# Performance work log

Hardware: AMD Instinct MI355X
Metric: run time of the kernel (lower is better)

The kernel has to match this reference:

```python
import jax, jax.numpy as jnp
import numpy as np

D = 128; T = 128; E = 100; H = 2
B = 2048; N0 = 3 * B; K0 = 5; N1 = N0 * K0; K1 = 10
NN = 200000; M = 4096; MSG = 2 * D + E + T  # 484


def t2v(t, w, b):
    # Time2Vec: cos(t * w + b), output [..., T]
    return jnp.cos(t[..., None] * w + b)


def gru_cell(x, h, Wih, bih, Whh, bhh):
    gi = x @ Wih.T + bih
    gh = h @ Whh.T + bhh
    ir, iz, inn = jnp.split(gi, 3, axis=-1)
    hr, hz, hn = jnp.split(gh, 3, axis=-1)
    r = jax.nn.sigmoid(ir + hr)
    u = jax.nn.sigmoid(iz + hz)
    n = jnp.tanh(inn + r * hn)
    return (1.0 - u) * n + u * h


def temporal_attn(node_feat, time_feat, edge_feat, nbr_feat, nbr_time_feat, mask,
                  Wq, bq, Wk, bk, Wv, bv, Wo, bo):
    N = node_feat.shape[0]
    q = (jnp.concatenate([node_feat, time_feat], -1) @ Wq + bq).reshape(N, H, D // H)
    kin = jnp.concatenate([nbr_feat, edge_feat, nbr_time_feat], -1)  # [N, K, D+E+T]
    k = (kin @ Wk + bk).reshape(N, -1, H, D // H)
    v = (kin @ Wv + bv).reshape(N, -1, H, D // H)
    s = jnp.einsum('nhd,nkhd->nhk', q, k) / jnp.sqrt(jnp.asarray(D // H, q.dtype))
    s = jnp.where(mask[:, None, :] > 0, s, jnp.asarray(-1e9, s.dtype))
    a = jax.nn.softmax(s, axis=-1)
    hout = jnp.einsum('nhk,nkhd->nhd', a, v).reshape(N, D)
    return jax.nn.relu(jnp.concatenate([hout, node_feat], -1) @ Wo + bo)


def setup_inputs() -> dict:
    key = jax.random.key(0)
    ks = jax.random.split(key, 60)
    it = iter(range(60))
    nx = lambda: ks[next(it)]
    p = lambda shape: jax.random.normal(nx(), shape, jnp.float32) * 0.05
    inp = dict(memory=p((NN, D)), time_w=p((T,)), time_b=p((T,)),
               gru_Wih=p((3 * D, MSG)), gru_bih=p((3 * D,)),
               gru_Whh=p((3 * D, D)), gru_bhh=p((3 * D,)))
    for l in (0, 1):
        inp['Wq%d' % l] = p((D + T, D)); inp['bq%d' % l] = p((D,))
        inp['Wk%d' % l] = p((D + E + T, D)); inp['bk%d' % l] = p((D,))
        inp['Wv%d' % l] = p((D + E + T, D)); inp['bv%d' % l] = p((D,))
        inp['Wo%d' % l] = p((2 * D, D)); inp['bo%d' % l] = p((D,))
    inp.update(lp_Ws=p((D, D)), lp_bs=p((D,)), lp_Wd=p((D, D)), lp_bd=p((D,)),
               lp_Wo=p((D, 1)), lp_bo=p((1,)))
    inp['msgs'] = jax.random.normal(nx(), (M, MSG), jnp.float32)
    inp['times0'] = jax.random.uniform(nx(), (N0,), jnp.float32) * 100.0 + 100.0
    inp['nbr_times0'] = inp['times0'][:, None] - jax.random.uniform(nx(), (N0, K0), jnp.float32) * 100.0
    inp['nbr_feats0'] = jax.random.normal(nx(), (N0, K0, E), jnp.float32)
    inp['times1'] = jax.random.uniform(nx(), (N1,), jnp.float32) * 100.0 + 100.0
    inp['nbr_times1'] = inp['times1'][:, None] - jax.random.uniform(nx(), (N1, K1), jnp.float32) * 100.0
    inp['nbr_feats1'] = jax.random.normal(nx(), (N1, K1, E), jnp.float32)
    inp['msg_nids'] = jax.random.permutation(nx(), NN)[:M].astype(jnp.int32)
    inp['seed0'] = jax.random.randint(nx(), (N0,), 0, NN, jnp.int32)
    inp['seed1'] = jax.random.randint(nx(), (N1,), 0, NN, jnp.int32)
    inp['nbr_local0'] = (N0 + jax.random.randint(nx(), (N0, K0), 0, N1)).astype(jnp.int32)
    inp['nbr_mask0'] = jax.random.randint(nx(), (N0, K0), 0, 2, jnp.int32).at[:, 0].set(1)
    inp['nbr_mask1'] = jax.random.randint(nx(), (N1, K1), 0, 2, jnp.int32).at[:, 0].set(1)
    inp['src_local'] = jax.random.randint(nx(), (B,), 0, N0, jnp.int32)
    inp['dst_local'] = jax.random.randint(nx(), (B,), 0, N0, jnp.int32)
    inp['neg_local'] = jax.random.randint(nx(), (B,), 0, N0, jnp.int32)
    return inp


def reference(memory, time_w, time_b, gru_Wih, gru_bih, gru_Whh, gru_bhh,
              Wq0, bq0, Wk0, bk0, Wv0, bv0, Wo0, bo0,
              Wq1, bq1, Wk1, bk1, Wv1, bv1, Wo1, bo1,
              lp_Ws, lp_bs, lp_Wd, lp_bd, lp_Wo, lp_bo,
              msgs, times0, nbr_times0, nbr_feats0, times1, nbr_times1, nbr_feats1,
              msg_nids, seed0, seed1, nbr_local0, nbr_mask0, nbr_mask1,
              src_local, dst_local, neg_local):
    # GRU memory update on aggregated messages (get_updated_memory)
    mem = memory.at[msg_nids].set(
        gru_cell(msgs, memory[msg_nids], gru_Wih, gru_bih, gru_Whh, gru_bhh))
    z = jnp.zeros((N0 + N1, D), jnp.float32)
    # hop 1 (outermost): neighbor node features are zeros
    tf1 = t2v(jnp.zeros((N1,), jnp.float32), time_w, time_b)
    ntf1 = t2v(times1[:, None] - nbr_times1, time_w, time_b)
    out1 = temporal_attn(mem[seed1], tf1, nbr_feats1,
                         jnp.zeros((N1, K1, D), jnp.float32), ntf1, nbr_mask1,
                         Wq1, bq1, Wk1, bk1, Wv1, bv1, Wo1, bo1)
    z = z.at[N0 + jnp.arange(N1)].set(out1)
    # hop 0: gather neighbor embeddings from hop-1 results
    tf0 = t2v(jnp.zeros((N0,), jnp.float32), time_w, time_b)
    ntf0 = t2v(times0[:, None] - nbr_times0, time_w, time_b)
    out0 = temporal_attn(mem[seed0], tf0, nbr_feats0, z[nbr_local0], ntf0, nbr_mask0,
                         Wq0, bq0, Wk0, bk0, Wv0, bv0, Wo0, bo0)
    z = z.at[jnp.arange(N0)].set(out0)
    z_src, z_dst, z_neg = z[src_local], z[dst_local], z[neg_local]

    def link_pred(a, c):
        hh = jax.nn.relu(a @ lp_Ws + lp_bs + c @ lp_Wd + lp_bd)
        return jax.nn.sigmoid(hh @ lp_Wo + lp_bo).ravel()

    return link_pred(z_src, z_dst), link_pred(z_src, z_neg)
```

## Files before the change

kernel.cpp:

```cpp
#include <hip/hip_runtime.h>
#include <math.h>

#define D    128
#define TT   128
#define E    100
#define NHD  2
#define BSZ  2048
#define N0C  6144
#define K0C  5
#define N1C  30720
#define K1C  10
#define NNC  200000
#define MC   4096
#define MSG  484
#define KIN  356
#define GK   612
#define GKP  616
#define GN   512

typedef __attribute__((ext_vector_type(8))) short short8v;
typedef __attribute__((ext_vector_type(4))) float f32x4;

__device__ __forceinline__ float sigmoidf_(float x){ return 1.f/(1.f+__expf(-x)); }
__device__ __forceinline__ unsigned short f2b(float f){
    unsigned int x = __float_as_uint(f);
    unsigned int r = (x + 0x7fffu + ((x>>16)&1u)) >> 16;
    return (unsigned short)r;
}
__device__ __forceinline__ float b2f(unsigned short u){
    return __uint_as_float(((unsigned int)u)<<16);
}

__global__ void k_pre_small(const float* time_b,
                            const float* Wq0,const float* bq0,const float* Wq1,const float* bq1,
                            const float* bv0,const float* Wo0,const float* bo0,
                            const float* bv1,const float* Wo1,const float* bo1,
                            float* qc0, float* qc1, float* cb0, float* cb1){
    __shared__ float cosb[TT];
    int j = threadIdx.x;
    cosb[j] = cosf(time_b[j]);
    __syncthreads();
    float a0=bq0[j], a1=bq1[j];
    for(int t=0;t<TT;++t){ a0 += cosb[t]*Wq0[(D+t)*D + j]; a1 += cosb[t]*Wq1[(D+t)*D + j]; }
    qc0[j]=a0; qc1[j]=a1;
    float c0=bo0[j], c1=bo1[j];
    for(int jp=0;jp<D;++jp){ c0 += bv0[jp]*Wo0[jp*D + j]; c1 += bv1[jp]*Wo1[jp*D + j]; }
    cb0[j]=c0; cb1[j]=c1;
}

__global__ void k_wf(const float* Wq,const float* Wk,const float* bk,const float* qc,
                     unsigned short* WF, float* cF, int cmin){
    int span = 356 - cmin;
    int hstr = span + 4;
    int width = 2*hstr;
    int idx = blockIdx.x;
    int h = idx / hstr; int cl = idx % hstr;
    int k = threadIdx.x;
    if(cl > span){
        WF[(size_t)k*width + idx] = (unsigned short)0;
        if(k==0) cF[idx] = 0.f;
        return;
    }
    int c = cmin + cl;
    float a = 0.f;
    for(int d=0; d<64; ++d){
        float wkv = (c < KIN) ? Wk[c*D + h*64+d] : bk[h*64+d];
        a += Wq[k*D + h*64+d] * wkv;
    }
    WF[(size_t)k*width + idx] = f2b(a);
    if(k==0){
        float s=0.f;
        for(int d=0; d<64; ++d){
            float wkv = (c < KIN) ? Wk[c*D + h*64+d] : bk[h*64+d];
            s += qc[h*64+d]*wkv;
        }
        cF[idx] = s;
    }
}

__global__ void k_bcat(const float* Wv, const float* Wo, unsigned short* Bcat, int cmin){
    int span = KIN - cmin; int rows = 2*span;
    int r = blockIdx.x; int j = threadIdx.x;
    float a;
    if(r < rows){
        int h = r/span; int c = cmin + (r - h*span);
        a = 0.f;
        for(int d=0; d<64; ++d) a += Wv[c*D + h*64+d] * Wo[(h*64+d)*D + j];
    } else {
        a = Wo[(size_t)(D + (r - rows))*D + j];
    }
    Bcat[(size_t)r*D + j] = f2b(a);
}

__global__ __launch_bounds__(256) void k_gruB(const float* Wih, const float* Whh, unsigned short* B){
    __shared__ float tile[64][65];
    int rb = blockIdx.x*64;
    int jb = blockIdx.y*64;
    int t = threadIdx.x;
    int rr = t&63, jj0 = t>>6;
    #pragma unroll
    for(int i=0;i<16;++i){
        int jj = jj0 + i*4;
        int j = jb + jj; int r = rb + rr;
        float v = 0.f;
        if(r < GK){
            if(j < 256)      v = (r<MSG)? Wih[(size_t)j*MSG+r] : Whh[(size_t)j*D + (r-MSG)];
            else if(j < 384) v = (r<MSG)? Wih[(size_t)j*MSG+r] : 0.f;
            else             v = (r<MSG)? 0.f : Whh[(size_t)(j-128)*D + (r-MSG)];
        }
        tile[jj][rr] = v;
    }
    __syncthreads();
    int jw = t&63, rr0 = t>>6;
    #pragma unroll
    for(int i=0;i<16;++i){
        int rr2 = rr0 + i*4;
        int r = rb + rr2;
        if(r < GK) B[(size_t)r*GN + jb + jw] = f2b(tile[jw][rr2]);
    }
}
__global__ void k_gruBias(const float* bih, const float* bhh, float* bias){
    int j = threadIdx.x + blockIdx.x*256;
    if(j >= GN) return;
    float v;
    if(j < 256)      v = bih[j] + bhh[j];
    else if(j < 384) v = bih[j];
    else             v = bhh[j-128];
    bias[j] = v;
}
__global__ void k_acvt(const float* msgs, const float* memory, const int* msg_nids,
                       unsigned short* ab, float* hprevf){
    int i = blockIdx.x*256 + threadIdx.x;
    if(i >= MC*GKP) return;
    int row = i / GKP; int c = i - row*GKP;
    float v;
    if(c < MSG) v = msgs[(size_t)row*MSG + c];
    else if(c < GK){ int d = c-MSG; v = memory[(size_t)msg_nids[row]*D + d]; hprevf[row*D+d] = v; }
    else v = 0.f;
    ab[i] = f2b(v);
}
__global__ void k_gates3(const float* part, const float* bias, const float* hprevf, float* upd){
    int i = blockIdx.x*256 + threadIdx.x;
    if(i >= MC*D) return;
    int row = i>>7, d = i&127;
    const float* p = part + (size_t)row*GN;
    const size_t S = (size_t)MC*GN;
    float gr = p[d]     + p[S+d]     + p[2*S+d]     + bias[d];
    float gu = p[128+d] + p[S+128+d] + p[2*S+128+d] + bias[128+d];
    float gi = p[256+d] + p[S+256+d] + p[2*S+256+d] + bias[256+d];
    float gh = p[384+d] + p[S+384+d] + p[2*S+384+d] + bias[384+d];
    float r = sigmoidf_(gr);
    float u = sigmoidf_(gu);
    float n = tanhf(gi + r*gh);
    upd[i] = (1.f-u)*n + u*hprevf[i];
}

__global__ void k_map_init(int* map){ int i = blockIdx.x*256+threadIdx.x; if(i<NNC) map[i] = -1; }
__global__ void k_map_scatter(const int* msg_nids, int* map){
    int i = blockIdx.x*256+threadIdx.x; if(i<MC) map[msg_nids[i]] = i;
}

__global__ void k_gatherf(const int* seed1,const int* seed0,const int* map,
                          const float* memory,const float* upd,
                          unsigned short* hb1, unsigned short* acat1,
                          unsigned short* hb0, unsigned short* acat0){
    int i = blockIdx.x*256 + threadIdx.x;
    const int total1 = N1C*D;
    int li; const int* seed; unsigned short* hb; unsigned short* acat; int ldav, hoff;
    if(i < total1){ li=i; seed=seed1; hb=hb1; acat=acat1; ldav=584; hoff=456; }
    else { li = i - total1; if(li >= N0C*D) return; seed=seed0; hb=hb0; acat=acat0; ldav=840; hoff=712; }
    int row = li>>7, c = li&127;
    int sid = seed[row];
    int mi = map[sid];
    float v = (mi>=0) ? upd[(size_t)mi*D + c] : memory[(size_t)sid*D + c];
    unsigned short u = f2b(v);
    hb[li] = u;
    acat[(size_t)row*ldav + hoff + c] = u;
}

template<int BM, int SPLITK, bool RELU, bool OUTF32>
__global__ __launch_bounds__(256) void k_gmm(const unsigned short* A, int lda,
                                             const unsigned short* B, int ldb,
                                             const float* bias, void* Cp, int ldc,
                                             int K, int N, int M){
    constexpr int ASTR = 72;
    constexpr int BSTR = 72;
    constexpr int RPW = BM/4;
    constexpr int RT  = RPW/16;
    constexpr int AIT = BM/32;
    __shared__ unsigned short As[BM*ASTR];
    __shared__ unsigned short Bs[64*BSTR];
    int t = threadIdx.x;
    int wave = t>>6, lane = t&63;
    int l15 = lane&15, l4 = lane>>4;
    int m0 = blockIdx.y*BM, n0 = blockIdx.x*64;
    int ntiles = (K+63)>>6;
    int tbeg, tend;
    if(SPLITK==1){ tbeg=0; tend=ntiles; }
    else {
        int tper = (ntiles + SPLITK-1)/SPLITK;
        tbeg = blockIdx.z*tper;
        tend = min(ntiles, tbeg+tper);
    }
    f32x4 acc[RT][4];
    #pragma unroll
    for(int rt=0;rt<RT;++rt)
        #pragma unroll
        for(int ct=0;ct<4;++ct) acc[rt][ct] = (f32x4){0.f,0.f,0.f,0.f};

    uint4 apre[AIT]; unsigned short bpre[16];
    auto loadA = [&](int kt){
        int k0 = kt<<6;
        #pragma unroll
        for(int i=0;i<AIT;++i){
            int idx = t + i*256;
            int row = idx>>3; int kc = (idx&7)*8;
            uint4 v = {0u,0u,0u,0u};
            if(k0+kc < K) v = *(const uint4*)(A + (size_t)(m0+row)*lda + k0 + kc);
            apre[i] = v;
        }
    };
    auto loadB = [&](int kt){
        int k0 = kt<<6;
        int n = t&63; int kb = (t>>6)*16;
        int ng = n0+n;
        #pragma unroll
        for(int j=0;j<16;++j){
            int kg = k0 + kb + j;
            bpre[j] = (kg<K && ng<N) ? B[(size_t)kg*ldb + ng] : (unsigned short)0;
        }
    };
    auto stash = [&](){
        #pragma unroll
        for(int i=0;i<AIT;++i){
            int idx = t + i*256;
            int row = idx>>3; int kc = (idx&7)*8;
            *(uint4*)&As[row*ASTR + kc] = apre[i];
        }
        int n = t&63; int kb = (t>>6)*16;
        #pragma unroll
        for(int j=0;j<16;++j) Bs[n*BSTR + kb + j] = bpre[j];
    };

    loadA(tbeg); loadB(tbeg);
    for(int kt=tbeg; kt<tend; ++kt){
        stash();
        __syncthreads();
        if(kt+1 < tend){ loadA(kt+1); loadB(kt+1); }
        #pragma unroll
        for(int kk=0; kk<64; kk+=32){
            short8v bfr[4];
            #pragma unroll
            for(int ct=0;ct<4;++ct)
                bfr[ct] = *(const short8v*)&Bs[(ct*16+l15)*BSTR + kk + l4*8];
            #pragma unroll
            for(int rt=0;rt<RT;++rt){
                short8v afr = *(const short8v*)&As[(wave*RPW + rt*16 + l15)*ASTR + kk + l4*8];
                #pragma unroll
                for(int ct=0;ct<4;++ct)
                    acc[rt][ct] = __builtin_amdgcn_mfma_f32_16x16x32_bf16(afr, bfr[ct], acc[rt][ct], 0,0,0);
            }
        }
        __syncthreads();
    }
    #pragma unroll
    for(int rt=0;rt<RT;++rt){
        #pragma unroll
        for(int ct=0;ct<4;++ct){
            int col = n0 + ct*16 + l15;
            if(col < N){
                #pragma unroll
                for(int r=0;r<4;++r){
                    int row = m0 + wave*RPW + rt*16 + l4*4 + r;
                    if(SPLITK==1){
                        float v = acc[rt][ct][r] + bias[col];
                        if(RELU) v = fmaxf(v, 0.f);
                        if(OUTF32) ((float*)Cp)[(size_t)row*ldc + col] = v;
                        else ((unsigned short*)Cp)[(size_t)row*ldc + col] = f2b(v);
                    } else {
                        ((float*)Cp)[((size_t)blockIdx.z*M + row)*ldc + col] = acc[rt][ct][r];
                    }
                }
            }
        }
    }
}

template<int SPL, bool RELU, bool OUTF32>
__global__ void k_kred(const float* part, int M, int N, const float* bias, void* out){
    int i = blockIdx.x*256 + threadIdx.x;
    if(i >= M*N) return;
    int col = i & (N-1);
    float v = bias[col];
    #pragma unroll
    for(int z=0;z<SPL;++z) v += part[(size_t)z*M*N + i];
    if(RELU) v = fmaxf(v, 0.f);
    if(OUTF32) ((float*)out)[i] = v;
    else ((unsigned short*)out)[i] = f2b(v);
}

template<int K, int CMIN, int S4, int NPW>
__global__ __launch_bounds__(256) void k_attn(const unsigned short* qwb,
    unsigned short* avout, int ldav,
    const float* times, const float* nbr_times, const float* nbr_feats,
    const int* nbr_mask, const int* nbr_local, const unsigned short* zbuf,
    const float* time_w, const float* time_b){
    constexpr int SPAN = KIN - CMIN;
    constexpr int QSTR = SPAN + 4;
    constexpr int QLD  = 2*QSTR;
    int wv = blockIdx.x*4 + (threadIdx.x>>6);
    int lane = threadIdx.x & 63;

    float4 tw4[S4], tb4[S4];
    #pragma unroll
    for(int s=0;s<S4;++s){
        int c = CMIN + s*256 + lane*4;
        if(c >= D+E && c < KIN){
            tw4[s] = *(const float4*)(time_w + (c-(D+E)));
            tb4[s] = *(const float4*)(time_b + (c-(D+E)));
        } else {
            tw4[s] = make_float4(0.f,0.f,0.f,0.f);
            tb4[s] = make_float4(0.f,0.f,0.f,0.f);
        }
    }

    for(int i=0;i<NPW;++i){
        int n = wv*NPW + i;
        const unsigned short* qrow = qwb + (size_t)n*QLD;
        float tval = (lane<K) ? nbr_times[(size_t)n*K + lane] : 0.f;
        int   mval = (lane<K) ? nbr_mask [(size_t)n*K + lane] : 0;
        int   nlv  = (CMIN==0 && lane<K) ? nbr_local[(size_t)n*K + lane] : 0;
        float tn = times[n];

        float4 qw4[NHD][S4]; float qb[NHD];
        #pragma unroll
        for(int h=0;h<NHD;++h){
            qb[h] = b2f(qrow[h*QSTR + SPAN]);
            #pragma unroll
            for(int s=0;s<S4;++s){
                int cl = s*256 + lane*4;
                float4 v = make_float4(0.f,0.f,0.f,0.f);
                if(cl < SPAN){
                    uint2 w = *(const uint2*)(qrow + h*QSTR + cl);
                    v.x = __uint_as_float(w.x<<16);
                    v.y = __uint_as_float(w.x & 0xffff0000u);
                    v.z = __uint_as_float(w.y<<16);
                    v.w = __uint_as_float(w.y & 0xffff0000u);
                }
                qw4[h][s] = v;
            }
        }

        float4 kin4[K][S4];
        float sval[NHD][K];
        unsigned int actmask = 0;
        #pragma unroll
        for(int k=0;k<K;++k){
            int mk = __shfl(mval, k);
            if(mk > 0){
                actmask |= (1u<<k);
                float dt = tn - __shfl(tval, k);
                const float* ef = nbr_feats + (size_t)(n*K+k)*E;
                const unsigned short* zf = (CMIN==0) ?
                    (zbuf + (size_t)(__shfl(nlv,k) - N0C)*D) : (const unsigned short*)0;
                float p0=0.f, p1=0.f;
                #pragma unroll
                for(int s=0;s<S4;++s){
                    int c = CMIN + s*256 + lane*4;
                    float4 kv = make_float4(0.f,0.f,0.f,0.f);
                    if(c < KIN){
                        if(CMIN==0 && c < D){
                            uint2 w = *(const uint2*)(zf + c);
                            kv.x = __uint_as_float(w.x<<16);
                            kv.y = __uint_as_float(w.x & 0xffff0000u);
                            kv.z = __uint_as_float(w.y<<16);
                            kv.w = __uint_as_float(w.y & 0xffff0000u);
                        } else if(c < D+E){
                            kv = *(const float4*)(ef + (c-D));
                        } else {
                            kv.x = __cosf(dt*tw4[s].x + tb4[s].x);
                            kv.y = __cosf(dt*tw4[s].y + tb4[s].y);
                            kv.z = __cosf(dt*tw4[s].z + tb4[s].z);
                            kv.w = __cosf(dt*tw4[s].w + tb4[s].w);
                        }
                    }
                    kin4[k][s] = kv;
                    p0 += kv.x*qw4[0][s].x + kv.y*qw4[0][s].y + kv.z*qw4[0][s].z + kv.w*qw4[0][s].w;
                    p1 += kv.x*qw4[1][s].x + kv.y*qw4[1][s].y + kv.z*qw4[1][s].z + kv.w*qw4[1][s].w;
                }
                #pragma unroll
                for(int off=32; off; off>>=1){ p0 += __shfl_xor(p0, off); p1 += __shfl_xor(p1, off); }
                sval[0][k] = (p0 + qb[0])*0.125f;
                sval[1][k] = (p1 + qb[1])*0.125f;
            } else {
                #pragma unroll
                for(int s=0;s<S4;++s) kin4[k][s] = make_float4(0.f,0.f,0.f,0.f);
                sval[0][k] = -1e9f;
                sval[1][k] = -1e9f;
            }
        }
        #pragma unroll
        for(int h=0;h<NHD;++h){
            float mx = -1e30f;
            #pragma unroll
            for(int k=0;k<K;++k) mx = fmaxf(mx, sval[h][k]);
            float z=0.f;
            #pragma unroll
            for(int k=0;k<K;++k){ float e = __expf(sval[h][k]-mx); sval[h][k]=e; z+=e; }
            float inv = 1.f/z;
            #pragma unroll
            for(int k=0;k<K;++k) sval[h][k]*=inv;
        }
        #pragma unroll
        for(int h=0;h<NHD;++h)
          #pragma unroll
          for(int s=0;s<S4;++s){
            int cl = s*256 + lane*4;
            if(cl < SPAN){
                float v0=0.f,v1=0.f,v2=0.f,v3=0.f;
                #pragma unroll
                for(int k=0;k<K;++k){
                    if(actmask & (1u<<k)){
                        float a = sval[h][k];
                        v0 += a*kin4[k][s].x; v1 += a*kin4[k][s].y;
                        v2 += a*kin4[k][s].z; v3 += a*kin4[k][s].w;
                    }
                }
                uint2 o;
                o.x = (unsigned int)f2b(v0) | ((unsigned int)f2b(v1)<<16);
                o.y = (unsigned int)f2b(v2) | ((unsigned int)f2b(v3)<<16);
                *(uint2*)(avout + (size_t)n*ldav + h*SPAN + cl) = o;
            }
          }
    }
}

__global__ __launch_bounds__(128) void k_linkpred(const float* z0,
      const int* src,const int* dst,const int* neg,
      const float* Ws,const float* bs,const float* Wd,const float* bd,
      const float* Wo,const float* bo, float* out){
    __shared__ float zs[D], zd[D], zn[D];
    __shared__ float red[4];
    int b = blockIdx.x; int d = threadIdx.x;
    zs[d] = z0[(size_t)src[b]*D + d];
    zd[d] = z0[(size_t)dst[b]*D + d];
    zn[d] = z0[(size_t)neg[b]*D + d];
    __syncthreads();
    float ss=0.f, sdd=0.f, snn=0.f;
    for(int c=0;c<D;++c){
        float w1 = Ws[c*D + d], w2 = Wd[c*D + d];
        ss  += zs[c]*w1; sdd += zd[c]*w2; snn += zn[c]*w2;
    }
    float bb = bs[d] + bd[d];
    float h1 = fmaxf(ss + sdd + bb, 0.f);
    float h2 = fmaxf(ss + snn + bb, 0.f);
    float w = Wo[d];
    float v1 = h1*w, v2 = h2*w;
    #pragma unroll
    for(int off=32; off; off>>=1){ v1 += __shfl_xor(v1,off); v2 += __shfl_xor(v2,off); }
    int wid = d>>6;
    if((d&63)==0){ red[wid*2]=v1; red[wid*2+1]=v2; }
    __syncthreads();
    if(d==0){
        out[b]       = sigmoidf_(red[0]+red[2] + bo[0]);
        out[BSZ + b] = sigmoidf_(red[1]+red[3] + bo[0]);
    }
}

extern "C" void kernel_launch(void* const* d_in, const int* in_sizes, int n_in,
                              void* d_out, int out_size, void* d_ws, size_t ws_size,
                              hipStream_t stream) {
    const float* memory  = (const float*)d_in[0];
    const float* time_w  = (const float*)d_in[1];
    const float* time_b  = (const float*)d_in[2];
    const float* gWih    = (const float*)d_in[3];
    const float* gbih    = (const float*)d_in[4];
    const float* gWhh    = (const float*)d_in[5];
    const float* gbhh    = (const float*)d_in[6];
    const float* Wq0=(const float*)d_in[7],  *bq0=(const float*)d_in[8];
    const float* Wk0=(const float*)d_in[9],  *bk0=(const float*)d_in[10];
    const float* Wv0=(const float*)d_in[11], *bv0=(const float*)d_in[12];
    const float* Wo0=(const float*)d_in[13], *bo0=(const float*)d_in[14];
    const float* Wq1=(const float*)d_in[15], *bq1=(const float*)d_in[16];
    const float* Wk1=(const float*)d_in[17], *bk1=(const float*)d_in[18];
    const float* Wv1=(const float*)d_in[19], *bv1=(const float*)d_in[20];
    const float* Wo1=(const float*)d_in[21], *bo1=(const float*)d_in[22];
    const float* lpWs=(const float*)d_in[23], *lpbs=(const float*)d_in[24];
    const float* lpWd=(const float*)d_in[25], *lpbd=(const float*)d_in[26];
    const float* lpWo=(const float*)d_in[27], *lpbo=(const float*)d_in[28];
    const float* msgs    = (const float*)d_in[29];
    const float* times0  = (const float*)d_in[30];
    const float* ntimes0 = (const float*)d_in[31];
    const float* nfeats0 = (const float*)d_in[32];
    const float* times1  = (const float*)d_in[33];
    const float* ntimes1 = (const float*)d_in[34];
    const float* nfeats1 = (const float*)d_in[35];
    const int* msg_nids  = (const int*)d_in[36];
    const int* seed0     = (const int*)d_in[37];
    const int* seed1     = (const int*)d_in[38];
    const int* nbr_local0= (const int*)d_in[39];
    const int* nbr_mask0 = (const int*)d_in[40];
    const int* nbr_mask1 = (const int*)d_in[41];
    const int* src       = (const int*)d_in[42];
    const int* dst       = (const int*)d_in[43];
    const int* neg       = (const int*)d_in[44];

    char* ws = (char*)d_ws;
    size_t off = 0;
    auto alloc = [&](size_t bytes)->char*{
        char* p = ws + off;
        off += (bytes + 255) & ~(size_t)255;
        return p;
    };
    int*   map   = (int*)  alloc((size_t)NNC*4);
    float* upd   = (float*)alloc((size_t)MC*D*4);
    unsigned short* hb1   = (unsigned short*)alloc((size_t)N1C*D*2);
    unsigned short* qwb1  = (unsigned short*)alloc((size_t)N1C*464*2);
    unsigned short* acat1 = (unsigned short*)alloc((size_t)N1C*584*2);
    unsigned short* zb1   = (unsigned short*)alloc((size_t)N1C*D*2);
    unsigned short* hb0   = (unsigned short*)alloc((size_t)N0C*D*2);
    unsigned short* qwb0  = (unsigned short*)alloc((size_t)N0C*720*2);
    unsigned short* acat0 = (unsigned short*)alloc((size_t)N0C*840*2);
    float* z0    = (float*)alloc((size_t)N0C*D*4);
    float* qc0   = (float*)alloc(512);
    float* qc1   = (float*)alloc(512);
    float* cb0   = (float*)alloc(512);
    float* cb1   = (float*)alloc(512);
    unsigned short* WFb0 = (unsigned short*)alloc((size_t)D*720*2);
    unsigned short* WFb1 = (unsigned short*)alloc((size_t)D*464*2);
    float* cF0   = (float*)alloc((size_t)720*4);
    float* cF1   = (float*)alloc((size_t)464*4);
    unsigned short* Bcat1 = (unsigned short*)alloc((size_t)584*D*2);
    unsigned short* Bcat0 = (unsigned short*)alloc((size_t)840*D*2);
    unsigned short* gA    = (unsigned short*)alloc((size_t)MC*GKP*2);
    unsigned short* gB    = (unsigned short*)alloc((size_t)GK*GN*2);
    float* gBias = (float*)alloc((size_t)GN*4);
    float* hprevf= (float*)alloc((size_t)MC*D*4);
    float* part  = (float*)alloc((size_t)2*N1C*D*4);
    float* outp = (float*)d_out;

    k_pre_small<<<1,128,0,stream>>>(time_b, Wq0,bq0,Wq1,bq1, bv0,Wo0,bo0, bv1,Wo1,bo1,
                                    qc0,qc1,cb0,cb1);
    k_wf<<<720,128,0,stream>>>(Wq0,Wk0,bk0,qc0, WFb0,cF0, 0);
    k_wf<<<464,128,0,stream>>>(Wq1,Wk1,bk1,qc1, WFb1,cF1, 128);
    k_bcat<<<584,128,0,stream>>>(Wv1, Wo1, Bcat1, 128);
    k_bcat<<<840,128,0,stream>>>(Wv0, Wo0, Bcat0, 0);
    k_gruB<<<dim3(10,8),256,0,stream>>>(gWih, gWhh, gB);
    k_gruBias<<<2,256,0,stream>>>(gbih, gbhh, gBias);

    k_map_init<<<(NNC+255)/256,256,0,stream>>>(map);
    k_map_scatter<<<MC/256,256,0,stream>>>(msg_nids, map);
    k_acvt<<<(MC*GKP+255)/256,256,0,stream>>>(msgs, memory, msg_nids, gA, hprevf);
    k_gmm<128,3,false,true><<<dim3(GN/64, MC/128, 3),256,0,stream>>>(gA,GKP, gB,GN, gBias, part,GN, GK, GN, MC);
    k_gates3<<<(MC*D+255)/256,256,0,stream>>>(part, gBias, hprevf, upd);

    k_gatherf<<<((N1C+N0C)*D)/256,256,0,stream>>>(seed1, seed0, map, memory, upd,
                                                  hb1, acat1, hb0, acat0);

    k_gmm<128,1,false,false><<<dim3(8,  N1C/128),256,0,stream>>>(hb1,128, WFb1,464, cF1, qwb1,464, 128, 464, N1C);
    k_gmm<128,1,false,false><<<dim3(12, N0C/128),256,0,stream>>>(hb0,128, WFb0,720, cF0, qwb0,720, 128, 720, N0C);

    k_attn<K1C,128,1,2><<<N1C/8,256,0,stream>>>(qwb1, acat1, 584, times1, ntimes1, nfeats1,
                                                nbr_mask1, (const int*)0, (const unsigned short*)0,
                                                time_w, time_b);
    k_gmm<128,2,true,false><<<dim3(2, N1C/128, 2),256,0,stream>>>(acat1,584, Bcat1,D, cb1, part,D, 584, D, N1C);
    k_kred<2,true,false><<<(N1C*D+255)/256,256,0,stream>>>(part, N1C, D, cb1, zb1);

    k_attn<K0C,0,2,1><<<N0C/4,256,0,stream>>>(qwb0, acat0, 840, times0, ntimes0, nfeats0,
                                              nbr_mask0, nbr_local0, zb1,
                                              time_w, time_b);
    k_gmm<64,4,true,true><<<dim3(2, N0C/64, 4),256,0,stream>>>(acat0,840, Bcat0,D, cb0, part,D, 840, D, N0C);
    k_kred<4,true,true><<<(N0C*D+255)/256,256,0,stream>>>(part, N0C, D, cb0, z0);

    k_linkpred<<<BSZ,128,0,stream>>>(z0, src,dst,neg, lpWs,lpbs,lpWd,lpbd, lpWo,lpbo, outp);
}
```

Measured before the change: 599.2 us.

## Batch neighbor loads and shuffle reductions in attention kernel, drop mask branches

Restructures the temporal attention kernel so that mask, time and neighbor-index values for all K neighbors are read up front. All key vectors are then gathered before the dot products, and the cross-lane reductions for every neighbor run together. Per-neighbor mask branches go away: masked neighbors are computed and then zeroed through the -1e9 softmax score. Hop 1 now uses one node per wave with twice the blocks; `__restrict__` and readfirstlane are added. The aim is more memory-level and instruction-level parallelism to hide gather latency, at the cost of more registers and extra loads for masked neighbors, whose indices may point to invalid memory.

```diff
diff --git a/kernel.cpp b/kernel.cpp
--- a/kernel.cpp
+++ b/kernel.cpp
@@ -300,15 +300,17 @@
 }
 
 template<int K, int CMIN, int S4, int NPW>
-__global__ __launch_bounds__(256) void k_attn(const unsigned short* qwb,
-    unsigned short* avout, int ldav,
-    const float* times, const float* nbr_times, const float* nbr_feats,
-    const int* nbr_mask, const int* nbr_local, const unsigned short* zbuf,
-    const float* time_w, const float* time_b){
+__global__ __launch_bounds__(256) void k_attn(const unsigned short* __restrict__ qwb,
+    unsigned short* __restrict__ avout, int ldav,
+    const float* __restrict__ times, const float* __restrict__ nbr_times,
+    const float* __restrict__ nbr_feats,
+    const int* __restrict__ nbr_mask, const int* __restrict__ nbr_local,
+    const unsigned short* __restrict__ zbuf,
+    const float* __restrict__ time_w, const float* __restrict__ time_b){
     constexpr int SPAN = KIN - CMIN;
     constexpr int QSTR = SPAN + 4;
     constexpr int QLD  = 2*QSTR;
-    int wv = blockIdx.x*4 + (threadIdx.x>>6);
+    int wv = __builtin_amdgcn_readfirstlane(blockIdx.x*4 + (threadIdx.x>>6));
     int lane = threadIdx.x & 63;
 
     float4 tw4[S4], tb4[S4];
@@ -324,13 +326,18 @@
         }
     }
 
+    #pragma unroll
     for(int i=0;i<NPW;++i){
         int n = wv*NPW + i;
         const unsigned short* qrow = qwb + (size_t)n*QLD;
-        float tval = (lane<K) ? nbr_times[(size_t)n*K + lane] : 0.f;
-        int   mval = (lane<K) ? nbr_mask [(size_t)n*K + lane] : 0;
-        int   nlv  = (CMIN==0 && lane<K) ? nbr_local[(size_t)n*K + lane] : 0;
         float tn = times[n];
+        int   mk[K]; float tk[K]; int nl[K];
+        #pragma unroll
+        for(int k=0;k<K;++k){
+            mk[k] = nbr_mask [(size_t)n*K + k];
+            tk[k] = nbr_times[(size_t)n*K + k];
+            nl[k] = (CMIN==0) ? nbr_local[(size_t)n*K + k] : 0;
+        }
 
         float4 qw4[NHD][S4]; float qb[NHD];
         #pragma unroll
@@ -352,52 +359,64 @@
         }
 
         float4 kin4[K][S4];
+        #pragma unroll
+        for(int k=0;k<K;++k){
+            float dt = tn - tk[k];
+            const float* ef = nbr_feats + (size_t)(n*K+k)*E;
+            const unsigned short* zf = (CMIN==0) ?
+                (zbuf + (size_t)(nl[k] - N0C)*D) : (const unsigned short*)0;
+            #pragma unroll
+            for(int s=0;s<S4;++s){
+                int c = CMIN + s*256 + lane*4;
+                float4 kv = make_float4(0.f,0.f,0.f,0.f);
+                if(c < KIN){
+                    if(CMIN==0 && c < D){
+                        uint2 w = *(const uint2*)(zf + c);
+                        kv.x = __uint_as_float(w.x<<16);
+                        kv.y = __uint_as_float(w.x & 0xffff0000u);
+                        kv.z = __uint_as_float(w.y<<16);
+                        kv.w = __uint_as_float(w.y & 0xffff0000u);
+                    } else if(c < D+E){
+                        kv = *(const float4*)(ef + (c-D));
+                    } else {
+                        kv.x = __cosf(dt*tw4[s].x + tb4[s].x);
+                        kv.y = __cosf(dt*tw4[s].y + tb4[s].y);
+                        kv.z = __cosf(dt*tw4[s].z + tb4[s].z);
+                        kv.w = __cosf(dt*tw4[s].w + tb4[s].w);
+                    }
+                }
+                kin4[k][s] = kv;
+            }
+        }
+
+        float p0[K], p1[K];
+        #pragma unroll
+        for(int k=0;k<K;++k){
+            float a0 = 0.f, a1 = 0.f;
+            #pragma unroll
+            for(int s=0;s<S4;++s){
+                float4 kv = kin4[k][s];
+                a0 += kv.x*qw4[0][s].x + kv.y*qw4[0][s].y + kv.z*qw4[0][s].z + kv.w*qw4[0][s].w;
+                a1 += kv.x*qw4[1][s].x + kv.y*qw4[1][s].y + kv.z*qw4[1][s].z + kv.w*qw4[1][s].w;
+            }
+            p0[k] = a0; p1[k] = a1;
+        }
+
+        #pragma unroll
+        for(int off=32; off; off>>=1){
+            #pragma unroll
+            for(int k=0;k<K;++k){
+                p0[k] += __shfl_xor(p0[k], off);
+                p1[k] += __shfl_xor(p1[k], off);
+            }
+        }
+
         float sval[NHD][K];
-        unsigned int actmask = 0;
         #pragma unroll
         for(int k=0;k<K;++k){
-            int mk = __shfl(mval, k);
-            if(mk > 0){
-                actmask |= (1u<<k);
-                float dt = tn - __shfl(tval, k);
-                const float* ef = nbr_feats + (size_t)(n*K+k)*E;
-                const unsigned short* zf = (CMIN==0) ?
-                    (zbuf + (size_t)(__shfl(nlv,k) - N0C)*D) : (const unsigned short*)0;
-                float p0=0.f, p1=0.f;
-                #pragma unroll
-                for(int s=0;s<S4;++s){
-                    int c = CMIN + s*256 + lane*4;
-                    float4 kv = make_float4(0.f,0.f,0.f,0.f);
-                    if(c < KIN){
-                        if(CMIN==0 && c < D){
-                            uint2 w = *(const uint2*)(zf + c);
-                            kv.x = __uint_as_float(w.x<<16);
-                            kv.y = __uint_as_float(w.x & 0xffff0000u);
-                            kv.z = __uint_as_float(w.y<<16);
-                            kv.w = __uint_as_float(w.y & 0xffff0000u);
-                        } else if(c < D+E){
-                            kv = *(const float4*)(ef + (c-D));
-                        } else {
-                            kv.x = __cosf(dt*tw4[s].x + tb4[s].x);
-                            kv.y = __cosf(dt*tw4[s].y + tb4[s].y);
-                            kv.z = __cosf(dt*tw4[s].z + tb4[s].z);
-                            kv.w = __cosf(dt*tw4[s].w + tb4[s].w);
-                        }
-                    }
-                    kin4[k][s] = kv;
-                    p0 += kv.x*qw4[0][s].x + kv.y*qw4[0][s].y + kv.z*qw4[0][s].z + kv.w*qw4[0][s].w;
-                    p1 += kv.x*qw4[1][s].x + kv.y*qw4[1][s].y + kv.z*qw4[1][s].z + kv.w*qw4[1][s].w;
-                }
-                #pragma unroll
-                for(int off=32; off; off>>=1){ p0 += __shfl_xor(p0, off); p1 += __shfl_xor(p1, off); }
-                sval[0][k] = (p0 + qb[0])*0.125f;
-                sval[1][k] = (p1 + qb[1])*0.125f;
-            } else {
-                #pragma unroll
-                for(int s=0;s<S4;++s) kin4[k][s] = make_float4(0.f,0.f,0.f,0.f);
-                sval[0][k] = -1e9f;
-                sval[1][k] = -1e9f;
-            }
+            bool act = mk[k] > 0;
+            sval[0][k] = act ? (p0[k] + qb[0])*0.125f : -1e9f;
+            sval[1][k] = act ? (p1[k] + qb[1])*0.125f : -1e9f;
         }
         #pragma unroll
         for(int h=0;h<NHD;++h){
@@ -420,11 +439,9 @@
                 float v0=0.f,v1=0.f,v2=0.f,v3=0.f;
                 #pragma unroll
                 for(int k=0;k<K;++k){
-                    if(actmask & (1u<<k)){
-                        float a = sval[h][k];
-                        v0 += a*kin4[k][s].x; v1 += a*kin4[k][s].y;
-                        v2 += a*kin4[k][s].z; v3 += a*kin4[k][s].w;
-                    }
+                    float a = sval[h][k];
+                    v0 += a*kin4[k][s].x; v1 += a*kin4[k][s].y;
+                    v2 += a*kin4[k][s].z; v3 += a*kin4[k][s].w;
                 }
                 uint2 o;
                 o.x = (unsigned int)f2b(v0) | ((unsigned int)f2b(v1)<<16);
@@ -560,7 +577,7 @@
     k_gmm<128,1,false,false><<<dim3(8,  N1C/128),256,0,stream>>>(hb1,128, WFb1,464, cF1, qwb1,464, 128, 464, N1C);
     k_gmm<128,1,false,false><<<dim3(12, N0C/128),256,0,stream>>>(hb0,128, WFb0,720, cF0, qwb0,720, 128, 720, N0C);
 
-    k_attn<K1C,128,1,2><<<N1C/8,256,0,stream>>>(qwb1, acat1, 584, times1, ntimes1, nfeats1,
+    k_attn<K1C,128,1,1><<<N1C/4,256,0,stream>>>(qwb1, acat1, 584, times1, ntimes1, nfeats1,
                                                 nbr_mask1, (const int*)0, (const unsigned short*)0,
                                                 time_w, time_b);
     k_gmm<128,2,true,false><<<dim3(2, N1C/128, 2),256,0,stream>>>(acat1,584, Bcat1,D, cb1, part,D, 584, D, N1C);
```

Result: faster. 559.0 us (-6.7%).
